# Kernel optimization log

Hardware: AMD Instinct MI355X
Metric: run time of the kernel (lower is better)

## Reference

```python
import jax, jax.numpy as jnp
import numpy as np

N, T, E, D, U = 32, 2048, 512, 1024, 256


def setup_inputs() -> dict:
    key = jax.random.key(0)
    ks = jax.random.split(key, 6)
    queries = jax.random.normal(ks[0], (N, 1, D), dtype=jnp.float32)
    prev = jax.random.uniform(ks[1], (N, T), dtype=jnp.float32)
    prev = prev / jnp.sum(prev, axis=1, keepdims=True)  # distribution-like initial alignment
    memory = jax.random.normal(ks[2], (N, T, E), dtype=jnp.float32)
    W_q = jax.random.normal(ks[3], (D, U), dtype=jnp.float32) * (1.0 / np.sqrt(D))
    W_k = jax.random.normal(ks[4], (E, U), dtype=jnp.float32) * (1.0 / np.sqrt(E))
    v = jax.random.uniform(ks[5], (U,), dtype=jnp.float32)
    return {"queries": queries, "previous_alignments": prev, "memory": memory,
            "W_q": W_q, "W_k": W_k, "v": v}


def safe_cumprod_exclusive(x):
    # exclusive cumprod via log-space cumsum, clamped like the torch original
    logsum = jnp.cumsum(jnp.log(jnp.clip(x, 1e-20, 1.0)), axis=1)  # [N,T]
    excl = jnp.concatenate([jnp.zeros_like(logsum[:, :1]), logsum], axis=1)[:, :-1]
    return jnp.exp(excl)


def reference(queries, previous_alignments, memory, W_q, W_k, v):
    # Bahdanau additive score (normalize=False path)
    proj_key = jnp.einsum('bte,eu->btu', memory, W_k)          # set_memory
    proj_q = jnp.einsum('bqd,du->bqu', queries, W_q)           # [N,1,U]
    weights = jnp.einsum('btu,u->bt', jnp.tanh(proj_q + proj_key), v)  # [N,T]
    p_choose = jax.nn.sigmoid(weights)
    # monotonic attention recursion in cumsum/cumprod form
    cumprod_1mp = safe_cumprod_exclusive(1.0 - p_choose)
    alignments = p_choose * cumprod_1mp * jnp.cumsum(
        previous_alignments / jnp.clip(cumprod_1mp, 1e-10, 1.0), axis=1)
    contexts = jnp.einsum('bt,bte->be', alignments, memory)    # bmm + squeeze
    return (contexts, alignments)
```

## Files before the change

### kernel.cpp

```cpp
#include <hip/hip_runtime.h>
#include <math.h>

#define N_ 32
#define T_ 2048
#define E_ 512
#define D_ 1024
#define U_ 256

typedef __attribute__((ext_vector_type(8))) short bf16x8;
typedef __attribute__((ext_vector_type(16))) float f32x16;

__device__ __forceinline__ short f2bf_rne(float x) {
  unsigned int u = __float_as_uint(x);
  unsigned int r = u + 0x7FFFu + ((u >> 16) & 1u);
  return (short)(r >> 16);
}
__device__ __forceinline__ short f2bf_trunc(float x) {
  return (short)(__float_as_uint(x) >> 16);
}
__device__ __forceinline__ float bf2f(short h) {
  return __uint_as_float(((unsigned int)(unsigned short)h) << 16);
}
__device__ __forceinline__ float fast_tanh(float x) {
  float t = exp2f(x * 2.8853900817779268f);
  return 1.0f - 2.0f * __builtin_amdgcn_rcpf(t + 1.0f);
}
__device__ __forceinline__ float fast_sigmoid(float w) {
  return __builtin_amdgcn_rcpf(1.0f + exp2f(-1.4426950408889634f * w));
}

__global__ __launch_bounds__(256) void prep_kernel(
    const float* __restrict__ Wk, const float* __restrict__ queries,
    const float* __restrict__ Wq, bf16x8* __restrict__ whiP,
    bf16x8* __restrict__ wloP, float* __restrict__ pq_part) {
  const int wg = blockIdx.x, tid = threadIdx.x;
  if (wg < 64) {
    const int fid = wg * 256 + tid;
    const int lane = fid & 63;
    const int ub = (fid >> 6) & 7;
    const int kc = (fid >> 9) & 3;
    const int c = fid >> 11;
    const int u = ub * 32 + (lane & 31);
    const int e0 = c * 64 + kc * 16 + (lane >> 5) * 8;
    bf16x8 H, L;
#pragma unroll
    for (int j = 0; j < 8; ++j) {
      float x = Wk[(size_t)(e0 + j) * U_ + u];
      short h = f2bf_trunc(x);
      H[j] = h;
      L[j] = f2bf_rne(x - bf2f(h));
    }
    whiP[fid] = H;
    wloP[fid] = L;
  } else {
    const int ch = (wg - 64) & 3;
    const int bb = (wg - 64) >> 2;
    const int d0 = ch * 256;
    const float* q = queries + bb * D_ + d0;
    const float* wq = Wq + (size_t)d0 * U_ + tid;
    float acc = 0.f;
#pragma unroll 8
    for (int d = 0; d < 256; ++d)
      acc = fmaf(q[d], wq[(size_t)d * U_], acc);
    pq_part[(bb * 4 + ch) * U_ + tid] = acc;
  }
}

__global__ __launch_bounds__(256, 2) void score_kernel(
    const float* __restrict__ memory, const bf16x8* __restrict__ whiP,
    const bf16x8* __restrict__ wloP, const float* __restrict__ pq_part,
    const float* __restrict__ v, float* __restrict__ p_choose) {
  __shared__ short sA[2][128 * 64];
  __shared__ float smem_w[4][128];

  const int b = blockIdx.y;
  const int t0 = blockIdx.x * 128;
  const int tid = threadIdx.x;
  const int lane = tid & 63;
  const int ty = tid >> 6;
  const int l31 = lane & 31;
  const int half = lane >> 5;

  f32x16 acc[4][2];
#pragma unroll
  for (int mt = 0; mt < 4; ++mt)
#pragma unroll
    for (int nt = 0; nt < 2; ++nt)
#pragma unroll
      for (int r = 0; r < 16; ++r) acc[mt][nt][r] = 0.f;

  const int sr = tid >> 1;
  const int cs = (tid & 1) * 16;
  const int s0 = cs >> 3;
  const int sw = sr & 7;
  const float* srow = memory + ((size_t)(b * T_ + t0 + sr)) * E_ + cs;
  char* const bp0 = (char*)&sA[0][0] + sr * 128;
  char* const bp1 = (char*)&sA[1][0] + sr * 128;

  float4 xr[4];
#pragma unroll
  for (int j = 0; j < 4; ++j) xr[j] = *(const float4*)(srow + j * 4);

  auto do_stage = [&](char* bp) {
    float xs[16] = {xr[0].x, xr[0].y, xr[0].z, xr[0].w,
                    xr[1].x, xr[1].y, xr[1].z, xr[1].w,
                    xr[2].x, xr[2].y, xr[2].z, xr[2].w,
                    xr[3].x, xr[3].y, xr[3].z, xr[3].w};
    bf16x8 H0, H1, L0, L1;
#pragma unroll
    for (int i = 0; i < 8; ++i) {
      short h0 = f2bf_trunc(xs[i]);
      H0[i] = h0;
      L0[i] = f2bf_rne(xs[i] - bf2f(h0));
      short h1 = f2bf_trunc(xs[8 + i]);
      H1[i] = h1;
      L1[i] = f2bf_rne(xs[8 + i] - bf2f(h1));
    }
    *(bf16x8*)(bp + (((s0 + 0) ^ sw) * 16)) = H0;
    *(bf16x8*)(bp + (((s0 + 1) ^ sw) * 16)) = H1;
    *(bf16x8*)(bp + (((s0 + 4) ^ sw) * 16)) = L0;
    *(bf16x8*)(bp + (((s0 + 5) ^ sw) * 16)) = L1;
  };

  do_stage(bp0);
  __syncthreads();

  int cur = 0;
  for (int it = 0; it < 16; ++it) {
    if (it < 15) {
      const float* src = srow + (it + 1) * 32;
#pragma unroll
      for (int j = 0; j < 4; ++j) xr[j] = *(const float4*)(src + j * 4);
    }
    const char* base = (const char*)&sA[cur][0];
#pragma unroll
    for (int kc = 0; kc < 2; ++kc) {
      bf16x8 bh[2], bl[2];
#pragma unroll
      for (int nt = 0; nt < 2; ++nt) {
        const int fidx = ((it * 2 + kc) * 8 + (ty * 2 + nt)) * 64 + lane;
        bh[nt] = whiP[fidx];
        bl[nt] = wloP[fidx];
      }
      const int sl = kc * 2 + half;
      bf16x8 ah[4], al[4];
#pragma unroll
      for (int mt = 0; mt < 4; ++mt) {
        const int m = mt * 32 + l31;
        ah[mt] = *(const bf16x8*)(base + (size_t)m * 128 + ((sl ^ (m & 7)) * 16));
        al[mt] = *(const bf16x8*)(base + (size_t)m * 128 + (((sl + 4) ^ (m & 7)) * 16));
      }
#pragma unroll
      for (int mt = 0; mt < 4; ++mt)
#pragma unroll
        for (int nt = 0; nt < 2; ++nt) {
          acc[mt][nt] = __builtin_amdgcn_mfma_f32_32x32x16_bf16(ah[mt], bh[nt], acc[mt][nt], 0, 0, 0);
          acc[mt][nt] = __builtin_amdgcn_mfma_f32_32x32x16_bf16(ah[mt], bl[nt], acc[mt][nt], 0, 0, 0);
          acc[mt][nt] = __builtin_amdgcn_mfma_f32_32x32x16_bf16(al[mt], bh[nt], acc[mt][nt], 0, 0, 0);
        }
    }
    if (it < 15) do_stage(cur ? bp0 : bp1);
    __syncthreads();
    cur ^= 1;
  }

  const int u0 = ty * 64 + l31;
  const int u1 = u0 + 32;
  float pq0 = 0.f, pq1 = 0.f;
#pragma unroll
  for (int c = 0; c < 4; ++c) {
    pq0 += pq_part[(b * 4 + c) * U_ + u0];
    pq1 += pq_part[(b * 4 + c) * U_ + u1];
  }
  const float v0 = v[u0], v1 = v[u1];
#pragma unroll
  for (int mt = 0; mt < 4; ++mt)
#pragma unroll
    for (int r = 0; r < 16; ++r) {
      float s = fast_tanh(acc[mt][0][r] + pq0) * v0 + fast_tanh(acc[mt][1][r] + pq1) * v1;
#pragma unroll
      for (int off = 1; off < 32; off <<= 1) s += __shfl_xor(s, off, 64);
      if (l31 == 0) {
        const int row = mt * 32 + (r & 3) + 8 * (r >> 2) + 4 * half;
        smem_w[ty][row] = s;
      }
    }
  __syncthreads();
  if (tid < 128) {
    const float w = smem_w[0][tid] + smem_w[1][tid] + smem_w[2][tid] + smem_w[3][tid];
    p_choose[b * T_ + t0 + tid] = fast_sigmoid(w);
  }
}

__device__ __forceinline__ float block_incl_scan(float val, float* sbuf, int tid) {
  float x = val;
  sbuf[tid] = x;
  __syncthreads();
#pragma unroll
  for (int off = 1; off < 256; off <<= 1) {
    float t = (tid >= off) ? sbuf[tid - off] : 0.f;
    __syncthreads();
    x += t;
    sbuf[tid] = x;
    __syncthreads();
  }
  return x;
}

__global__ __launch_bounds__(256) void scan_kernel(
    const float* __restrict__ p_choose, const float* __restrict__ prev,
    float* __restrict__ align_out, float* __restrict__ ctx_out) {
  __shared__ float sbuf[256];
  const int b = blockIdx.x, tid = threadIdx.x;
  ctx_out[b * E_ + tid] = 0.f;
  ctx_out[b * E_ + 256 + tid] = 0.f;
  const int base = b * T_ + tid * 8;
  float4 p0 = *(const float4*)(p_choose + base);
  float4 p1 = *(const float4*)(p_choose + base + 4);
  float p[8] = {p0.x, p0.y, p0.z, p0.w, p1.x, p1.y, p1.z, p1.w};
  float s[8];
  float run = 0.f;
#pragma unroll
  for (int k = 0; k < 8; ++k) {
    float x = 1.0f - p[k];
    x = fminf(fmaxf(x, 1e-20f), 1.0f);
    run += logf(x);
    s[k] = run;
  }
  float incl = block_incl_scan(run, sbuf, tid);
  float excl = incl - run;
  float cp[8];
#pragma unroll
  for (int k = 0; k < 8; ++k)
    cp[k] = expf(excl + (k ? s[k - 1] : 0.f));
  float4 r0 = *(const float4*)(prev + base);
  float4 r1 = *(const float4*)(prev + base + 4);
  float pr[8] = {r0.x, r0.y, r0.z, r0.w, r1.x, r1.y, r1.z, r1.w};
  float s2[8];
  float run2 = 0.f;
#pragma unroll
  for (int k = 0; k < 8; ++k) {
    float d = fminf(fmaxf(cp[k], 1e-10f), 1.0f);
    run2 += pr[k] / d;
    s2[k] = run2;
  }
  float incl2 = block_incl_scan(run2, sbuf, tid);
  float excl2 = incl2 - run2;
#pragma unroll
  for (int k = 0; k < 8; ++k)
    p[k] = p[k] * cp[k] * (excl2 + s2[k]);
  *(float4*)(align_out + base) = make_float4(p[0], p[1], p[2], p[3]);
  *(float4*)(align_out + base + 4) = make_float4(p[4], p[5], p[6], p[7]);
}

__global__ __launch_bounds__(256) void ctx_kernel(
    const float* __restrict__ memory, const float* __restrict__ align,
    float* __restrict__ ctx_out) {
  const int wg = blockIdx.x, tid = threadIdx.x;
  const int b = wg >> 4;
  const int t0 = (wg & 15) * 128 + (tid >> 7) * 64;
  const int col = (tid & 127) * 4;
  const float* mrow = memory + ((size_t)(b * T_ + t0)) * E_ + col;
  const float* arow = align + b * T_ + t0;
  float4 a = make_float4(0.f, 0.f, 0.f, 0.f);
  for (int t = 0; t < 64; t += 4) {
    float4 m0 = *(const float4*)(mrow + (size_t)(t + 0) * E_);
    float4 m1 = *(const float4*)(mrow + (size_t)(t + 1) * E_);
    float4 m2 = *(const float4*)(mrow + (size_t)(t + 2) * E_);
    float4 m3 = *(const float4*)(mrow + (size_t)(t + 3) * E_);
    float a0 = arow[t], a1 = arow[t + 1], a2 = arow[t + 2], a3 = arow[t + 3];
    a.x = fmaf(a0, m0.x, a.x); a.y = fmaf(a0, m0.y, a.y);
    a.z = fmaf(a0, m0.z, a.z); a.w = fmaf(a0, m0.w, a.w);
    a.x = fmaf(a1, m1.x, a.x); a.y = fmaf(a1, m1.y, a.y);
    a.z = fmaf(a1, m1.z, a.z); a.w = fmaf(a1, m1.w, a.w);
    a.x = fmaf(a2, m2.x, a.x); a.y = fmaf(a2, m2.y, a.y);
    a.z = fmaf(a2, m2.z, a.z); a.w = fmaf(a2, m2.w, a.w);
    a.x = fmaf(a3, m3.x, a.x); a.y = fmaf(a3, m3.y, a.y);
    a.z = fmaf(a3, m3.z, a.z); a.w = fmaf(a3, m3.w, a.w);
  }
  float* dst = ctx_out + b * E_ + col;
  atomicAdd(dst + 0, a.x);
  atomicAdd(dst + 1, a.y);
  atomicAdd(dst + 2, a.z);
  atomicAdd(dst + 3, a.w);
}

extern "C" void kernel_launch(void* const* d_in, const int* in_sizes, int n_in,
                              void* d_out, int out_size, void* d_ws, size_t ws_size,
                              hipStream_t stream) {
  (void)in_sizes; (void)n_in; (void)out_size; (void)ws_size;
  const float* queries = (const float*)d_in[0];
  const float* prev    = (const float*)d_in[1];
  const float* memory  = (const float*)d_in[2];
  const float* Wq      = (const float*)d_in[3];
  const float* Wk      = (const float*)d_in[4];
  const float* v       = (const float*)d_in[5];

  float* out = (float*)d_out;
  float* ctx_out = out;
  float* align_out = out + N_ * E_;

  float* ws = (float*)d_ws;
  bf16x8* whiP    = (bf16x8*)ws;
  bf16x8* wloP    = (bf16x8*)(ws + 65536);
  float* p_choose = ws + 131072;
  float* pq_part  = ws + 196608;

  prep_kernel<<<dim3(64 + 128), 256, 0, stream>>>(Wk, queries, Wq, whiP, wloP, pq_part);
  score_kernel<<<dim3(T_ / 128, N_), 256, 0, stream>>>(memory, whiP, wloP, pq_part, v, p_choose);
  scan_kernel<<<dim3(N_), 256, 0, stream>>>(p_choose, prev, align_out, ctx_out);
  ctx_kernel<<<dim3(512), 256, 0, stream>>>(memory, align_out, ctx_out);
}
```

Baseline: 268.8 us.

## Fuse four kernels into one cooperative persistent kernel with grid syncs

Merges the prep, score, scan and context kernels into a single cooperative launch of 256 blocks of 512 threads. Each block acts as two 256-thread virtual workgroups, and grid.sync separates the phases. This removes three kernel launch boundaries and their inter-kernel gaps. The cost is that the scan phase keeps only 32 virtual groups busy while the rest wait at the barrier, plus extra register and LDS pressure from the doubled block size, which could lower occupancy.

Result: slower. 464.6 us (+72.9%).

```diff
diff --git a/kernel.cpp b/kernel.cpp
--- a/kernel.cpp
+++ b/kernel.cpp
@@ -1,5 +1,8 @@
 #include <hip/hip_runtime.h>
+#include <hip/hip_cooperative_groups.h>
 #include <math.h>
+
+namespace cg = cooperative_groups;
 
 #define N_ 32
 #define T_ 2048
@@ -29,13 +32,39 @@
   return __builtin_amdgcn_rcpf(1.0f + exp2f(-1.4426950408889634f * w));
 }
 
-__global__ __launch_bounds__(256) void prep_kernel(
-    const float* __restrict__ Wk, const float* __restrict__ queries,
-    const float* __restrict__ Wq, bf16x8* __restrict__ whiP,
-    bf16x8* __restrict__ wloP, float* __restrict__ pq_part) {
-  const int wg = blockIdx.x, tid = threadIdx.x;
-  if (wg < 64) {
-    const int fid = wg * 256 + tid;
+__device__ __forceinline__ float block_incl_scan(float val, float* sbuf, int vtid) {
+  float x = val;
+  sbuf[vtid] = x;
+  __syncthreads();
+#pragma unroll
+  for (int off = 1; off < 256; off <<= 1) {
+    float t = (vtid >= off) ? sbuf[vtid - off] : 0.f;
+    __syncthreads();
+    x += t;
+    sbuf[vtid] = x;
+    __syncthreads();
+  }
+  return x;
+}
+
+__global__ __launch_bounds__(512, 2) void fused_kernel(
+    const float* __restrict__ queries, const float* __restrict__ prev,
+    const float* __restrict__ memory, const float* __restrict__ Wq,
+    const float* __restrict__ Wk, const float* __restrict__ v,
+    float* __restrict__ ctx_out, float* __restrict__ align_out,
+    bf16x8* __restrict__ whiP, bf16x8* __restrict__ wloP,
+    float* __restrict__ p_choose, float* __restrict__ pq_part) {
+  __shared__ short sA[2][2][128 * 64];
+  __shared__ float smem_w[2][4][128];
+
+  cg::grid_group grid = cg::this_grid();
+  const int tid = threadIdx.x;
+  const int sub = tid >> 8;
+  const int vtid = tid & 255;
+  const int vwg = blockIdx.x * 2 + sub;
+
+  if (vwg < 64) {
+    const int fid = vwg * 256 + vtid;
     const int lane = fid & 63;
     const int ub = (fid >> 6) & 7;
     const int kc = (fid >> 9) & 3;
@@ -52,237 +81,220 @@
     }
     whiP[fid] = H;
     wloP[fid] = L;
-  } else {
-    const int ch = (wg - 64) & 3;
-    const int bb = (wg - 64) >> 2;
+  } else if (vwg < 192) {
+    const int ch = (vwg - 64) & 3;
+    const int bb = (vwg - 64) >> 2;
     const int d0 = ch * 256;
     const float* q = queries + bb * D_ + d0;
-    const float* wq = Wq + (size_t)d0 * U_ + tid;
+    const float* wqp = Wq + (size_t)d0 * U_ + vtid;
     float acc = 0.f;
 #pragma unroll 8
     for (int d = 0; d < 256; ++d)
-      acc = fmaf(q[d], wq[(size_t)d * U_], acc);
-    pq_part[(bb * 4 + ch) * U_ + tid] = acc;
-  }
-}
-
-__global__ __launch_bounds__(256, 2) void score_kernel(
-    const float* __restrict__ memory, const bf16x8* __restrict__ whiP,
-    const bf16x8* __restrict__ wloP, const float* __restrict__ pq_part,
-    const float* __restrict__ v, float* __restrict__ p_choose) {
-  __shared__ short sA[2][128 * 64];
-  __shared__ float smem_w[4][128];
-
-  const int b = blockIdx.y;
-  const int t0 = blockIdx.x * 128;
-  const int tid = threadIdx.x;
-  const int lane = tid & 63;
-  const int ty = tid >> 6;
-  const int l31 = lane & 31;
-  const int half = lane >> 5;
-
-  f32x16 acc[4][2];
-#pragma unroll
-  for (int mt = 0; mt < 4; ++mt)
-#pragma unroll
-    for (int nt = 0; nt < 2; ++nt)
-#pragma unroll
-      for (int r = 0; r < 16; ++r) acc[mt][nt][r] = 0.f;
-
-  const int sr = tid >> 1;
-  const int cs = (tid & 1) * 16;
-  const int s0 = cs >> 3;
-  const int sw = sr & 7;
-  const float* srow = memory + ((size_t)(b * T_ + t0 + sr)) * E_ + cs;
-  char* const bp0 = (char*)&sA[0][0] + sr * 128;
-  char* const bp1 = (char*)&sA[1][0] + sr * 128;
-
-  float4 xr[4];
-#pragma unroll
-  for (int j = 0; j < 4; ++j) xr[j] = *(const float4*)(srow + j * 4);
-
-  auto do_stage = [&](char* bp) {
-    float xs[16] = {xr[0].x, xr[0].y, xr[0].z, xr[0].w,
-                    xr[1].x, xr[1].y, xr[1].z, xr[1].w,
-                    xr[2].x, xr[2].y, xr[2].z, xr[2].w,
-                    xr[3].x, xr[3].y, xr[3].z, xr[3].w};
-    bf16x8 H0, H1, L0, L1;
-#pragma unroll
-    for (int i = 0; i < 8; ++i) {
-      short h0 = f2bf_trunc(xs[i]);
-      H0[i] = h0;
-      L0[i] = f2bf_rne(xs[i] - bf2f(h0));
-      short h1 = f2bf_trunc(xs[8 + i]);
-      H1[i] = h1;
-      L1[i] = f2bf_rne(xs[8 + i] - bf2f(h1));
-    }
-    *(bf16x8*)(bp + (((s0 + 0) ^ sw) * 16)) = H0;
-    *(bf16x8*)(bp + (((s0 + 1) ^ sw) * 16)) = H1;
-    *(bf16x8*)(bp + (((s0 + 4) ^ sw) * 16)) = L0;
-    *(bf16x8*)(bp + (((s0 + 5) ^ sw) * 16)) = L1;
-  };
-
-  do_stage(bp0);
-  __syncthreads();
-
-  int cur = 0;
-  for (int it = 0; it < 16; ++it) {
-    if (it < 15) {
-      const float* src = srow + (it + 1) * 32;
-#pragma unroll
-      for (int j = 0; j < 4; ++j) xr[j] = *(const float4*)(src + j * 4);
-    }
-    const char* base = (const char*)&sA[cur][0];
-#pragma unroll
-    for (int kc = 0; kc < 2; ++kc) {
-      bf16x8 bh[2], bl[2];
-#pragma unroll
-      for (int nt = 0; nt < 2; ++nt) {
-        const int fidx = ((it * 2 + kc) * 8 + (ty * 2 + nt)) * 64 + lane;
-        bh[nt] = whiP[fidx];
-        bl[nt] = wloP[fidx];
+      acc = fmaf(q[d], wqp[(size_t)d * U_], acc);
+    pq_part[(bb * 4 + ch) * U_ + vtid] = acc;
+  }
+
+  __threadfence();
+  grid.sync();
+
+  {
+    const int b = vwg >> 4;
+    const int t0 = (vwg & 15) * 128;
+    const int lane = vtid & 63;
+    const int ty = vtid >> 6;
+    const int l31 = lane & 31;
+    const int half = lane >> 5;
+
+    f32x16 acc[4][2];
+#pragma unroll
+    for (int mt = 0; mt < 4; ++mt)
+#pragma unroll
+      for (int nt = 0; nt < 2; ++nt)
+#pragma unroll
+        for (int r = 0; r < 16; ++r) acc[mt][nt][r] = 0.f;
+
+    const int sr = vtid >> 1;
+    const int cs = (vtid & 1) * 16;
+    const int s0 = cs >> 3;
+    const int sw = sr & 7;
+    const float* srow = memory + ((size_t)(b * T_ + t0 + sr)) * E_ + cs;
+    char* const bp0 = (char*)&sA[sub][0][0] + sr * 128;
+    char* const bp1 = (char*)&sA[sub][1][0] + sr * 128;
+
+    float4 xr[4];
+#pragma unroll
+    for (int j = 0; j < 4; ++j) xr[j] = *(const float4*)(srow + j * 4);
+
+    auto do_stage = [&](char* bp) {
+      float xs[16] = {xr[0].x, xr[0].y, xr[0].z, xr[0].w,
+                      xr[1].x, xr[1].y, xr[1].z, xr[1].w,
+                      xr[2].x, xr[2].y, xr[2].z, xr[2].w,
+                      xr[3].x, xr[3].y, xr[3].z, xr[3].w};
+      bf16x8 H0, H1, L0, L1;
+#pragma unroll
+      for (int i = 0; i < 8; ++i) {
+        short h0 = f2bf_trunc(xs[i]);
+        H0[i] = h0;
+        L0[i] = f2bf_rne(xs[i] - bf2f(h0));
+        short h1 = f2bf_trunc(xs[8 + i]);
+        H1[i] = h1;
+        L1[i] = f2bf_rne(xs[8 + i] - bf2f(h1));
       }
-      const int sl = kc * 2 + half;
-      bf16x8 ah[4], al[4];
-#pragma unroll
-      for (int mt = 0; mt < 4; ++mt) {
-        const int m = mt * 32 + l31;
-        ah[mt] = *(const bf16x8*)(base + (size_t)m * 128 + ((sl ^ (m & 7)) * 16));
-        al[mt] = *(const bf16x8*)(base + (size_t)m * 128 + (((sl + 4) ^ (m & 7)) * 16));
+      *(bf16x8*)(bp + (((s0 + 0) ^ sw) * 16)) = H0;
+      *(bf16x8*)(bp + (((s0 + 1) ^ sw) * 16)) = H1;
+      *(bf16x8*)(bp + (((s0 + 4) ^ sw) * 16)) = L0;
+      *(bf16x8*)(bp + (((s0 + 5) ^ sw) * 16)) = L1;
+    };
+
+    do_stage(bp0);
+    __syncthreads();
+
+    int cur = 0;
+    for (int it = 0; it < 16; ++it) {
+      if (it < 15) {
+        const float* src = srow + (it + 1) * 32;
+#pragma unroll
+        for (int j = 0; j < 4; ++j) xr[j] = *(const float4*)(src + j * 4);
       }
-#pragma unroll
-      for (int mt = 0; mt < 4; ++mt)
+      const char* base = (const char*)&sA[sub][cur][0];
+#pragma unroll
+      for (int kc = 0; kc < 2; ++kc) {
+        bf16x8 bh[2], bl[2];
 #pragma unroll
         for (int nt = 0; nt < 2; ++nt) {
-          acc[mt][nt] = __builtin_amdgcn_mfma_f32_32x32x16_bf16(ah[mt], bh[nt], acc[mt][nt], 0, 0, 0);
-          acc[mt][nt] = __builtin_amdgcn_mfma_f32_32x32x16_bf16(ah[mt], bl[nt], acc[mt][nt], 0, 0, 0);
-          acc[mt][nt] = __builtin_amdgcn_mfma_f32_32x32x16_bf16(al[mt], bh[nt], acc[mt][nt], 0, 0, 0);
+          const int fidx = ((it * 2 + kc) * 8 + (ty * 2 + nt)) * 64 + lane;
+          bh[nt] = whiP[fidx];
+          bl[nt] = wloP[fidx];
         }
-    }
-    if (it < 15) do_stage(cur ? bp0 : bp1);
+        const int sl = kc * 2 + half;
+        bf16x8 ah[4], al[4];
+#pragma unroll
+        for (int mt = 0; mt < 4; ++mt) {
+          const int m = mt * 32 + l31;
+          ah[mt] = *(const bf16x8*)(base + (size_t)m * 128 + ((sl ^ (m & 7)) * 16));
+          al[mt] = *(const bf16x8*)(base + (size_t)m * 128 + (((sl + 4) ^ (m & 7)) * 16));
+        }
+#pragma unroll
+        for (int mt = 0; mt < 4; ++mt)
+#pragma unroll
+          for (int nt = 0; nt < 2; ++nt) {
+            acc[mt][nt] = __builtin_amdgcn_mfma_f32_32x32x16_bf16(ah[mt], bh[nt], acc[mt][nt], 0, 0, 0);
+            acc[mt][nt] = __builtin_amdgcn_mfma_f32_32x32x16_bf16(ah[mt], bl[nt], acc[mt][nt], 0, 0, 0);
+            acc[mt][nt] = __builtin_amdgcn_mfma_f32_32x32x16_bf16(al[mt], bh[nt], acc[mt][nt], 0, 0, 0);
+          }
+      }
+      if (it < 15) do_stage(cur ? bp0 : bp1);
+      __syncthreads();
+      cur ^= 1;
+    }
+
+    const int u0 = ty * 64 + l31;
+    const int u1 = u0 + 32;
+    float pq0 = 0.f, pq1 = 0.f;
+#pragma unroll
+    for (int c = 0; c < 4; ++c) {
+      pq0 += pq_part[(b * 4 + c) * U_ + u0];
+      pq1 += pq_part[(b * 4 + c) * U_ + u1];
+    }
+    const float v0 = v[u0], v1 = v[u1];
+#pragma unroll
+    for (int mt = 0; mt < 4; ++mt)
+#pragma unroll
+      for (int r = 0; r < 16; ++r) {
+        float s = fast_tanh(acc[mt][0][r] + pq0) * v0 + fast_tanh(acc[mt][1][r] + pq1) * v1;
+#pragma unroll
+        for (int off = 1; off < 32; off <<= 1) s += __shfl_xor(s, off, 64);
+        if (l31 == 0) {
+          const int row = mt * 32 + (r & 3) + 8 * (r >> 2) + 4 * half;
+          smem_w[sub][ty][row] = s;
+        }
+      }
     __syncthreads();
-    cur ^= 1;
-  }
-
-  const int u0 = ty * 64 + l31;
-  const int u1 = u0 + 32;
-  float pq0 = 0.f, pq1 = 0.f;
-#pragma unroll
-  for (int c = 0; c < 4; ++c) {
-    pq0 += pq_part[(b * 4 + c) * U_ + u0];
-    pq1 += pq_part[(b * 4 + c) * U_ + u1];
-  }
-  const float v0 = v[u0], v1 = v[u1];
-#pragma unroll
-  for (int mt = 0; mt < 4; ++mt)
-#pragma unroll
-    for (int r = 0; r < 16; ++r) {
-      float s = fast_tanh(acc[mt][0][r] + pq0) * v0 + fast_tanh(acc[mt][1][r] + pq1) * v1;
-#pragma unroll
-      for (int off = 1; off < 32; off <<= 1) s += __shfl_xor(s, off, 64);
-      if (l31 == 0) {
-        const int row = mt * 32 + (r & 3) + 8 * (r >> 2) + 4 * half;
-        smem_w[ty][row] = s;
-      }
-    }
-  __syncthreads();
-  if (tid < 128) {
-    const float w = smem_w[0][tid] + smem_w[1][tid] + smem_w[2][tid] + smem_w[3][tid];
-    p_choose[b * T_ + t0 + tid] = fast_sigmoid(w);
-  }
-}
-
-__device__ __forceinline__ float block_incl_scan(float val, float* sbuf, int tid) {
-  float x = val;
-  sbuf[tid] = x;
-  __syncthreads();
-#pragma unroll
-  for (int off = 1; off < 256; off <<= 1) {
-    float t = (tid >= off) ? sbuf[tid - off] : 0.f;
-    __syncthreads();
-    x += t;
-    sbuf[tid] = x;
-    __syncthreads();
-  }
-  return x;
-}
-
-__global__ __launch_bounds__(256) void scan_kernel(
-    const float* __restrict__ p_choose, const float* __restrict__ prev,
-    float* __restrict__ align_out, float* __restrict__ ctx_out) {
-  __shared__ float sbuf[256];
-  const int b = blockIdx.x, tid = threadIdx.x;
-  ctx_out[b * E_ + tid] = 0.f;
-  ctx_out[b * E_ + 256 + tid] = 0.f;
-  const int base = b * T_ + tid * 8;
-  float4 p0 = *(const float4*)(p_choose + base);
-  float4 p1 = *(const float4*)(p_choose + base + 4);
-  float p[8] = {p0.x, p0.y, p0.z, p0.w, p1.x, p1.y, p1.z, p1.w};
-  float s[8];
-  float run = 0.f;
-#pragma unroll
-  for (int k = 0; k < 8; ++k) {
-    float x = 1.0f - p[k];
-    x = fminf(fmaxf(x, 1e-20f), 1.0f);
-    run += logf(x);
-    s[k] = run;
-  }
-  float incl = block_incl_scan(run, sbuf, tid);
-  float excl = incl - run;
-  float cp[8];
-#pragma unroll
-  for (int k = 0; k < 8; ++k)
-    cp[k] = expf(excl + (k ? s[k - 1] : 0.f));
-  float4 r0 = *(const float4*)(prev + base);
-  float4 r1 = *(const float4*)(prev + base + 4);
-  float pr[8] = {r0.x, r0.y, r0.z, r0.w, r1.x, r1.y, r1.z, r1.w};
-  float s2[8];
-  float run2 = 0.f;
-#pragma unroll
-  for (int k = 0; k < 8; ++k) {
-    float d = fminf(fmaxf(cp[k], 1e-10f), 1.0f);
-    run2 += pr[k] / d;
-    s2[k] = run2;
-  }
-  float incl2 = block_incl_scan(run2, sbuf, tid);
-  float excl2 = incl2 - run2;
-#pragma unroll
-  for (int k = 0; k < 8; ++k)
-    p[k] = p[k] * cp[k] * (excl2 + s2[k]);
-  *(float4*)(align_out + base) = make_float4(p[0], p[1], p[2], p[3]);
-  *(float4*)(align_out + base + 4) = make_float4(p[4], p[5], p[6], p[7]);
-}
-
-__global__ __launch_bounds__(256) void ctx_kernel(
-    const float* __restrict__ memory, const float* __restrict__ align,
-    float* __restrict__ ctx_out) {
-  const int wg = blockIdx.x, tid = threadIdx.x;
-  const int b = wg >> 4;
-  const int t0 = (wg & 15) * 128 + (tid >> 7) * 64;
-  const int col = (tid & 127) * 4;
-  const float* mrow = memory + ((size_t)(b * T_ + t0)) * E_ + col;
-  const float* arow = align + b * T_ + t0;
-  float4 a = make_float4(0.f, 0.f, 0.f, 0.f);
-  for (int t = 0; t < 64; t += 4) {
-    float4 m0 = *(const float4*)(mrow + (size_t)(t + 0) * E_);
-    float4 m1 = *(const float4*)(mrow + (size_t)(t + 1) * E_);
-    float4 m2 = *(const float4*)(mrow + (size_t)(t + 2) * E_);
-    float4 m3 = *(const float4*)(mrow + (size_t)(t + 3) * E_);
-    float a0 = arow[t], a1 = arow[t + 1], a2 = arow[t + 2], a3 = arow[t + 3];
-    a.x = fmaf(a0, m0.x, a.x); a.y = fmaf(a0, m0.y, a.y);
-    a.z = fmaf(a0, m0.z, a.z); a.w = fmaf(a0, m0.w, a.w);
-    a.x = fmaf(a1, m1.x, a.x); a.y = fmaf(a1, m1.y, a.y);
-    a.z = fmaf(a1, m1.z, a.z); a.w = fmaf(a1, m1.w, a.w);
-    a.x = fmaf(a2, m2.x, a.x); a.y = fmaf(a2, m2.y, a.y);
-    a.z = fmaf(a2, m2.z, a.z); a.w = fmaf(a2, m2.w, a.w);
-    a.x = fmaf(a3, m3.x, a.x); a.y = fmaf(a3, m3.y, a.y);
-    a.z = fmaf(a3, m3.z, a.z); a.w = fmaf(a3, m3.w, a.w);
-  }
-  float* dst = ctx_out + b * E_ + col;
-  atomicAdd(dst + 0, a.x);
-  atomicAdd(dst + 1, a.y);
-  atomicAdd(dst + 2, a.z);
-  atomicAdd(dst + 3, a.w);
+    if (vtid < 128) {
+      const float w = smem_w[sub][0][vtid] + smem_w[sub][1][vtid] +
+                      smem_w[sub][2][vtid] + smem_w[sub][3][vtid];
+      p_choose[b * T_ + t0 + vtid] = fast_sigmoid(w);
+    }
+  }
+
+  __threadfence();
+  grid.sync();
+
+  if (vwg < 32) {
+    float* sbuf = &smem_w[sub][0][0];
+    const int b = vwg;
+    ctx_out[b * E_ + vtid] = 0.f;
+    ctx_out[b * E_ + 256 + vtid] = 0.f;
+    const int base = b * T_ + vtid * 8;
+    float4 p0 = *(const float4*)(p_choose + base);
+    float4 p1 = *(const float4*)(p_choose + base + 4);
+    float p[8] = {p0.x, p0.y, p0.z, p0.w, p1.x, p1.y, p1.z, p1.w};
+    float s[8];
+    float run = 0.f;
+#pragma unroll
+    for (int k = 0; k < 8; ++k) {
+      float x = 1.0f - p[k];
+      x = fminf(fmaxf(x, 1e-20f), 1.0f);
+      run += logf(x);
+      s[k] = run;
+    }
+    float incl = block_incl_scan(run, sbuf, vtid);
+    float excl = incl - run;
+    float cp[8];
+#pragma unroll
+    for (int k = 0; k < 8; ++k)
+      cp[k] = expf(excl + (k ? s[k - 1] : 0.f));
+    float4 r0 = *(const float4*)(prev + base);
+    float4 r1 = *(const float4*)(prev + base + 4);
+    float pr[8] = {r0.x, r0.y, r0.z, r0.w, r1.x, r1.y, r1.z, r1.w};
+    float s2[8];
+    float run2 = 0.f;
+#pragma unroll
+    for (int k = 0; k < 8; ++k) {
+      float d = fminf(fmaxf(cp[k], 1e-10f), 1.0f);
+      run2 += pr[k] / d;
+      s2[k] = run2;
+    }
+    float incl2 = block_incl_scan(run2, sbuf, vtid);
+    float excl2 = incl2 - run2;
+#pragma unroll
+    for (int k = 0; k < 8; ++k)
+      p[k] = p[k] * cp[k] * (excl2 + s2[k]);
+    *(float4*)(align_out + base) = make_float4(p[0], p[1], p[2], p[3]);
+    *(float4*)(align_out + base + 4) = make_float4(p[4], p[5], p[6], p[7]);
+  }
+
+  __threadfence();
+  grid.sync();
+
+  {
+    const int b = vwg >> 4;
+    const int t0 = (vwg & 15) * 128 + (vtid >> 7) * 64;
+    const int col = (vtid & 127) * 4;
+    const float* mrow = memory + ((size_t)(b * T_ + t0)) * E_ + col;
+    const float* arow = align_out + b * T_ + t0;
+    float4 a = make_float4(0.f, 0.f, 0.f, 0.f);
+    for (int t = 0; t < 64; t += 4) {
+      float4 m0 = *(const float4*)(mrow + (size_t)(t + 0) * E_);
+      float4 m1 = *(const float4*)(mrow + (size_t)(t + 1) * E_);
+      float4 m2 = *(const float4*)(mrow + (size_t)(t + 2) * E_);
+      float4 m3 = *(const float4*)(mrow + (size_t)(t + 3) * E_);
+      float a0 = arow[t], a1 = arow[t + 1], a2 = arow[t + 2], a3 = arow[t + 3];
+      a.x = fmaf(a0, m0.x, a.x); a.y = fmaf(a0, m0.y, a.y);
+      a.z = fmaf(a0, m0.z, a.z); a.w = fmaf(a0, m0.w, a.w);
+      a.x = fmaf(a1, m1.x, a.x); a.y = fmaf(a1, m1.y, a.y);
+      a.z = fmaf(a1, m1.z, a.z); a.w = fmaf(a1, m1.w, a.w);
+      a.x = fmaf(a2, m2.x, a.x); a.y = fmaf(a2, m2.y, a.y);
+      a.z = fmaf(a2, m2.z, a.z); a.w = fmaf(a2, m2.w, a.w);
+      a.x = fmaf(a3, m3.x, a.x); a.y = fmaf(a3, m3.y, a.y);
+      a.z = fmaf(a3, m3.z, a.z); a.w = fmaf(a3, m3.w, a.w);
+    }
+    float* dst = ctx_out + b * E_ + col;
+    atomicAdd(dst + 0, a.x);
+    atomicAdd(dst + 1, a.y);
+    atomicAdd(dst + 2, a.z);
+    atomicAdd(dst + 3, a.w);
+  }
 }
 
 extern "C" void kernel_launch(void* const* d_in, const int* in_sizes, int n_in,
@@ -306,8 +318,9 @@
   float* p_choose = ws + 131072;
   float* pq_part  = ws + 196608;
 
-  prep_kernel<<<dim3(64 + 128), 256, 0, stream>>>(Wk, queries, Wq, whiP, wloP, pq_part);
-  score_kernel<<<dim3(T_ / 128, N_), 256, 0, stream>>>(memory, whiP, wloP, pq_part, v, p_choose);
-  scan_kernel<<<dim3(N_), 256, 0, stream>>>(p_choose, prev, align_out, ctx_out);
-  ctx_kernel<<<dim3(512), 256, 0, stream>>>(memory, align_out, ctx_out);
-}
+  void* args[] = {(void*)&queries, (void*)&prev, (void*)&memory, (void*)&Wq,
+                  (void*)&Wk, (void*)&v, (void*)&ctx_out, (void*)&align_out,
+                  (void*)&whiP, (void*)&wloP, (void*)&p_choose, (void*)&pq_part};
+  hipLaunchCooperativeKernel((const void*)fused_kernel, dim3(256), dim3(512),
+                             args, 0, stream);
+}
```
